# Optimization experiments

Hardware: AMD Instinct MI355X
Metric: run time of the kernel (lower is better)

Reference implementation:

```python
import jax, jax.numpy as jnp
from jax import lax
import numpy as np

B, CIN, COUT, H, W = 32, 64, 64, 128, 128
KH = KW = 1
STRIDE = (1, 1)
PADDING = ((0, 0), (0, 0))


def setup_inputs() -> dict:
    key = jax.random.key(0)
    k1, k2, k3, k4 = jax.random.split(key, 4)
    x_quant = jax.random.randint(k1, (B, CIN, H, W), 0, 256, dtype=jnp.int32)  # uint8 values
    weight_int8 = jax.random.randint(k2, (COUT, CIN, KH, KW), -127, 128, dtype=jnp.int32)
    weight_scale = jax.random.uniform(k3, (COUT, 1, 1, 1), dtype=jnp.float32, minval=0.001, maxval=0.02)
    weight_zero_point = jnp.zeros((COUT, 1, 1, 1), dtype=jnp.int32)
    bias_fp32 = jax.random.normal(k4, (COUT,), dtype=jnp.float32) * 0.1
    return {
        "x_quant": x_quant,
        "input_scale": jnp.float32(0.02),
        "input_zero_point": jnp.int32(128),
        "weight_int8": weight_int8,
        "weight_scale": weight_scale,
        "weight_zero_point": weight_zero_point,
        "bias_fp32": bias_fp32,
        "output_scale": jnp.float32(0.05),
        "output_zero_point": jnp.int32(128),
    }


def reference(x_quant, input_scale, input_zero_point, weight_int8, weight_scale,
              weight_zero_point, bias_fp32, output_scale, output_zero_point):
    # dequant (zero-point subtract) in fp32
    x = x_quant.astype(jnp.float32) - input_zero_point.astype(jnp.float32)          # [B,Cin,H,W]
    w = weight_int8.astype(jnp.float32) - weight_zero_point.astype(jnp.float32)     # [O,I,kh,kw]
    conv = lax.conv_general_dilated(
        x, w, window_strides=STRIDE, padding=PADDING,
        dimension_numbers=("NCHW", "OIHW", "NCHW"))                                 # [B,O,H',W']
    # requantize: per-out-channel scale + bias, round, clamp to uint8 range
    requant_scale = (input_scale * weight_scale / output_scale).reshape(1, COUT, 1, 1)
    bias_term = (bias_fp32 / output_scale).reshape(1, COUT, 1, 1)
    final_float = conv * requant_scale + bias_term
    requant = jnp.round(final_float) + output_zero_point.astype(jnp.float32)
    out_q = jnp.clip(requant, 0.0, 255.0).astype(jnp.uint8)
    return out_q
```

## Files before the change

### kernel.cpp

```cpp
#include <hip/hip_runtime.h>

#define CIN   64
#define COUT  64
#define HW    16384
#define NPIX  (32 * HW)

__global__ void prep_kernel(const int* __restrict__ w,
                            const float* __restrict__ wscale,
                            const int* __restrict__ wzp,
                            const float* __restrict__ bias,
                            const float* __restrict__ is_p,
                            const float* __restrict__ os_p,
                            const int* __restrict__ ozp_p,
                            int* __restrict__ wp,
                            float4* __restrict__ params) {
    int o = threadIdx.x;
    if (o >= COUT) return;
    int zp = wzp[o];
    int sum = 0;
    #pragma unroll
    for (int k = 0; k < 16; ++k) {
        int c0 = w[o * CIN + 4 * k + 0] - zp;
        int c1 = w[o * CIN + 4 * k + 1] - zp;
        int c2 = w[o * CIN + 4 * k + 2] - zp;
        int c3 = w[o * CIN + 4 * k + 3] - zp;
        sum += c0 + c1 + c2 + c3;
        wp[o * 16 + k] = (c0 & 0xff) | ((c1 & 0xff) << 8) |
                         ((c2 & 0xff) << 16) | ((c3 & 0xff) << 24);
    }
    float scale = is_p[0] * wscale[o] / os_p[0];
    float bterm = bias[o] / os_p[0] + (float)ozp_p[0];
    float4 pr;
    pr.x = scale;
    pr.y = bterm;
    pr.z = __int_as_float(sum);
    pr.w = 0.0f;
    params[o] = pr;
}

__global__ __launch_bounds__(256) void conv_kernel(
    const int* __restrict__ x,
    const int* __restrict__ wp_g,
    const float4* __restrict__ params_g,
    const int* __restrict__ izp_p,
    int* __restrict__ out) {

    __shared__ int4  s_wp[COUT * 4];
    __shared__ float4 s_par[COUT];

    int tid = threadIdx.x;
    s_wp[tid] = ((const int4*)wp_g)[tid];
    if (tid < COUT) s_par[tid] = params_g[tid];
    int izp_adj = izp_p[0] - 128;
    __syncthreads();

    int t  = blockIdx.x * 256 + tid;
    int g4 = t * 4;
    int b  = g4 >> 14;
    int p  = g4 & (HW - 1);

    const int* xb = x + b * (CIN * HW) + p;

    int px[4][16];
    #pragma unroll
    for (int cg = 0; cg < 16; ++cg) {
        int4 v0 = *(const int4*)(xb + (4 * cg + 0) * HW);
        int4 v1 = *(const int4*)(xb + (4 * cg + 1) * HW);
        int4 v2 = *(const int4*)(xb + (4 * cg + 2) * HW);
        int4 v3 = *(const int4*)(xb + (4 * cg + 3) * HW);
        px[0][cg] = (v0.x | (v1.x << 8) | (v2.x << 16) | (v3.x << 24)) ^ 0x80808080;
        px[1][cg] = (v0.y | (v1.y << 8) | (v2.y << 16) | (v3.y << 24)) ^ 0x80808080;
        px[2][cg] = (v0.z | (v1.z << 8) | (v2.z << 16) | (v3.z << 24)) ^ 0x80808080;
        px[3][cg] = (v0.w | (v1.w << 8) | (v2.w << 16) | (v3.w << 24)) ^ 0x80808080;
    }

    int* ob = out + b * (COUT * HW) + p;

    #pragma unroll 2
    for (int o = 0; o < COUT; ++o) {
        int4 w0 = s_wp[o * 4 + 0];
        int4 w1 = s_wp[o * 4 + 1];
        int4 w2 = s_wp[o * 4 + 2];
        int4 w3 = s_wp[o * 4 + 3];
        float4 pr = s_par[o];
        int wsum = __float_as_int(pr.z);
        int base = -izp_adj * wsum;

        int4 r;
        #pragma unroll
        for (int j = 0; j < 4; ++j) {
            int acc = base;
            acc = __builtin_amdgcn_sdot4(px[j][0],  w0.x, acc, false);
            acc = __builtin_amdgcn_sdot4(px[j][1],  w0.y, acc, false);
            acc = __builtin_amdgcn_sdot4(px[j][2],  w0.z, acc, false);
            acc = __builtin_amdgcn_sdot4(px[j][3],  w0.w, acc, false);
            acc = __builtin_amdgcn_sdot4(px[j][4],  w1.x, acc, false);
            acc = __builtin_amdgcn_sdot4(px[j][5],  w1.y, acc, false);
            acc = __builtin_amdgcn_sdot4(px[j][6],  w1.z, acc, false);
            acc = __builtin_amdgcn_sdot4(px[j][7],  w1.w, acc, false);
            acc = __builtin_amdgcn_sdot4(px[j][8],  w2.x, acc, false);
            acc = __builtin_amdgcn_sdot4(px[j][9],  w2.y, acc, false);
            acc = __builtin_amdgcn_sdot4(px[j][10], w2.z, acc, false);
            acc = __builtin_amdgcn_sdot4(px[j][11], w2.w, acc, false);
            acc = __builtin_amdgcn_sdot4(px[j][12], w3.x, acc, false);
            acc = __builtin_amdgcn_sdot4(px[j][13], w3.y, acc, false);
            acc = __builtin_amdgcn_sdot4(px[j][14], w3.z, acc, false);
            acc = __builtin_amdgcn_sdot4(px[j][15], w3.w, acc, false);
            float f = fmaf((float)acc, pr.x, pr.y);
            f = rintf(f);
            f = fminf(fmaxf(f, 0.0f), 255.0f);
            (&r.x)[j] = (int)f;
        }
        *(int4*)(ob + o * HW) = r;
    }
}

extern "C" void kernel_launch(void* const* d_in, const int* in_sizes, int n_in,
                              void* d_out, int out_size, void* d_ws, size_t ws_size,
                              hipStream_t stream) {
    const int*   x      = (const int*)d_in[0];
    const float* is_p   = (const float*)d_in[1];
    const int*   izp_p  = (const int*)d_in[2];
    const int*   w      = (const int*)d_in[3];
    const float* wscale = (const float*)d_in[4];
    const int*   wzp    = (const int*)d_in[5];
    const float* bias   = (const float*)d_in[6];
    const float* os_p   = (const float*)d_in[7];
    const int*   ozp_p  = (const int*)d_in[8];

    int* out = (int*)d_out;

    int*    wp     = (int*)d_ws;
    float4* params = (float4*)((char*)d_ws + 4096);

    prep_kernel<<<1, 64, 0, stream>>>(w, wscale, wzp, bias, is_p, os_p, ozp_p, wp, params);

    conv_kernel<<<512, 256, 0, stream>>>(x, wp, params, izp_p, out);
}
```

Baseline: 270.9 us.

## Map one pixel per thread with scalar loads and nontemporal stores

Each thread now handles a single pixel instead of four, and the grid grows from 512 to 2048 blocks. Input loads become scalar dword loads that stay coalesced across the wavefront. Output writes use nontemporal stores, and the output-channel loop is unrolled by eight. The aim is more waves in flight and lower register pressure to hide memory latency in this bandwidth-bound kernel, at the cost of narrower memory transactions and more shared-memory weight reads per pixel.

```diff
diff --git a/kernel.cpp b/kernel.cpp
--- a/kernel.cpp
+++ b/kernel.cpp
@@ -54,29 +54,25 @@
     int izp_adj = izp_p[0] - 128;
     __syncthreads();
 
-    int t  = blockIdx.x * 256 + tid;
-    int g4 = t * 4;
-    int b  = g4 >> 14;
-    int p  = g4 & (HW - 1);
+    int t = blockIdx.x * 256 + tid;
+    int b = t >> 14;
+    int p = t & (HW - 1);
 
     const int* xb = x + b * (CIN * HW) + p;
 
-    int px[4][16];
+    int px[16];
     #pragma unroll
     for (int cg = 0; cg < 16; ++cg) {
-        int4 v0 = *(const int4*)(xb + (4 * cg + 0) * HW);
-        int4 v1 = *(const int4*)(xb + (4 * cg + 1) * HW);
-        int4 v2 = *(const int4*)(xb + (4 * cg + 2) * HW);
-        int4 v3 = *(const int4*)(xb + (4 * cg + 3) * HW);
-        px[0][cg] = (v0.x | (v1.x << 8) | (v2.x << 16) | (v3.x << 24)) ^ 0x80808080;
-        px[1][cg] = (v0.y | (v1.y << 8) | (v2.y << 16) | (v3.y << 24)) ^ 0x80808080;
-        px[2][cg] = (v0.z | (v1.z << 8) | (v2.z << 16) | (v3.z << 24)) ^ 0x80808080;
-        px[3][cg] = (v0.w | (v1.w << 8) | (v2.w << 16) | (v3.w << 24)) ^ 0x80808080;
+        int v0 = xb[(4 * cg + 0) * HW];
+        int v1 = xb[(4 * cg + 1) * HW];
+        int v2 = xb[(4 * cg + 2) * HW];
+        int v3 = xb[(4 * cg + 3) * HW];
+        px[cg] = (v0 | (v1 << 8) | (v2 << 16) | (v3 << 24)) ^ 0x80808080;
     }
 
     int* ob = out + b * (COUT * HW) + p;
 
-    #pragma unroll 2
+    #pragma unroll 8
     for (int o = 0; o < COUT; ++o) {
         int4 w0 = s_wp[o * 4 + 0];
         int4 w1 = s_wp[o * 4 + 1];
@@ -84,34 +80,29 @@
         int4 w3 = s_wp[o * 4 + 3];
         float4 pr = s_par[o];
         int wsum = __float_as_int(pr.z);
-        int base = -izp_adj * wsum;
+        int acc = -izp_adj * wsum;
 
-        int4 r;
-        #pragma unroll
-        for (int j = 0; j < 4; ++j) {
-            int acc = base;
-            acc = __builtin_amdgcn_sdot4(px[j][0],  w0.x, acc, false);
-            acc = __builtin_amdgcn_sdot4(px[j][1],  w0.y, acc, false);
-            acc = __builtin_amdgcn_sdot4(px[j][2],  w0.z, acc, false);
-            acc = __builtin_amdgcn_sdot4(px[j][3],  w0.w, acc, false);
-            acc = __builtin_amdgcn_sdot4(px[j][4],  w1.x, acc, false);
-            acc = __builtin_amdgcn_sdot4(px[j][5],  w1.y, acc, false);
-            acc = __builtin_amdgcn_sdot4(px[j][6],  w1.z, acc, false);
-            acc = __builtin_amdgcn_sdot4(px[j][7],  w1.w, acc, false);
-            acc = __builtin_amdgcn_sdot4(px[j][8],  w2.x, acc, false);
-            acc = __builtin_amdgcn_sdot4(px[j][9],  w2.y, acc, false);
-            acc = __builtin_amdgcn_sdot4(px[j][10], w2.z, acc, false);
-            acc = __builtin_amdgcn_sdot4(px[j][11], w2.w, acc, false);
-            acc = __builtin_amdgcn_sdot4(px[j][12], w3.x, acc, false);
-            acc = __builtin_amdgcn_sdot4(px[j][13], w3.y, acc, false);
-            acc = __builtin_amdgcn_sdot4(px[j][14], w3.z, acc, false);
-            acc = __builtin_amdgcn_sdot4(px[j][15], w3.w, acc, false);
-            float f = fmaf((float)acc, pr.x, pr.y);
-            f = rintf(f);
-            f = fminf(fmaxf(f, 0.0f), 255.0f);
-            (&r.x)[j] = (int)f;
-        }
-        *(int4*)(ob + o * HW) = r;
+        acc = __builtin_amdgcn_sdot4(px[0],  w0.x, acc, false);
+        acc = __builtin_amdgcn_sdot4(px[1],  w0.y, acc, false);
+        acc = __builtin_amdgcn_sdot4(px[2],  w0.z, acc, false);
+        acc = __builtin_amdgcn_sdot4(px[3],  w0.w, acc, false);
+        acc = __builtin_amdgcn_sdot4(px[4],  w1.x, acc, false);
+        acc = __builtin_amdgcn_sdot4(px[5],  w1.y, acc, false);
+        acc = __builtin_amdgcn_sdot4(px[6],  w1.z, acc, false);
+        acc = __builtin_amdgcn_sdot4(px[7],  w1.w, acc, false);
+        acc = __builtin_amdgcn_sdot4(px[8],  w2.x, acc, false);
+        acc = __builtin_amdgcn_sdot4(px[9],  w2.y, acc, false);
+        acc = __builtin_amdgcn_sdot4(px[10], w2.z, acc, false);
+        acc = __builtin_amdgcn_sdot4(px[11], w2.w, acc, false);
+        acc = __builtin_amdgcn_sdot4(px[12], w3.x, acc, false);
+        acc = __builtin_amdgcn_sdot4(px[13], w3.y, acc, false);
+        acc = __builtin_amdgcn_sdot4(px[14], w3.z, acc, false);
+        acc = __builtin_amdgcn_sdot4(px[15], w3.w, acc, false);
+
+        float f = fmaf((float)acc, pr.x, pr.y);
+        f = rintf(f);
+        f = fminf(fmaxf(f, 0.0f), 255.0f);
+        __builtin_nontemporal_store((int)f, ob + o * HW);
     }
 }
 
@@ -135,5 +126,5 @@
 
     prep_kernel<<<1, 64, 0, stream>>>(w, wscale, wzp, bias, is_p, os_p, ozp_p, wp, params);
 
-    conv_kernel<<<512, 256, 0, stream>>>(x, wp, params, izp_p, out);
+    conv_kernel<<<2048, 256, 0, stream>>>(x, wp, params, izp_p, out);
 }
```

Result: faster. 253.3 us (-6.5%).
